# Kernel optimization log

Hardware: AMD Instinct MI355X
Metric: run time of the kernel (lower is better)

The kernel has to match this reference:

```python
import jax, jax.numpy as jnp
import numpy as np

ENERGY_PERCENT = 0.8


def setup_inputs() -> dict:
    key = jax.random.key(0)
    B, T, C = 32, 4096, 128
    x = jax.random.normal(key, (B, T, C), dtype=jnp.float32)
    return {"x": x}


def reference(x):
    # x: [B, T, C]; FFT along time axis.
    T = x.shape[1]
    xf = jnp.fft.rfft(x, axis=1)                      # [B, F, C] complex
    energies = jnp.abs(xf) ** 2                       # [B, F, C]

    # Sort energies descending along freq axis (per batch, per channel).
    sorted_indices = jnp.argsort(-energies, axis=1)   # [B, F, C] int
    sorted_energies = jnp.take_along_axis(energies, sorted_indices, axis=1)

    total_energy = jnp.sum(energies, axis=1, keepdims=True)        # [B, 1, C]
    cumulative = jnp.cumsum(sorted_energies, axis=1)               # [B, F, C]

    # Smallest k such that cumulative energy exceeds energy_percent of total.
    exceeded = cumulative > total_energy * ENERGY_PERCENT          # [B, F, C] bool
    k = jnp.argmax(exceeded, axis=1) + 1                           # [B, C]

    # rank[b, f, c] = position of frequency f in the descending energy order;
    # this is the inverse permutation of sorted_indices (argsort of a permutation).
    rank = jnp.argsort(sorted_indices, axis=1)                     # [B, F, C]

    is_low_freq = rank < k[:, None, :]                             # [B, F, C]

    # Zero out the high-energy ("low-frequency") components -> residual x_var.
    mask = jnp.where(is_low_freq, 0.0, 1.0).astype(x.dtype)        # [B, F, C]
    x_var = jnp.fft.irfft(xf * mask, n=T, axis=1)                  # [B, T, C]
    x_inv = x - x_var
    return (x_var, x_inv)
```

## Files before the change

kernel.cpp:

```cpp
#include <hip/hip_runtime.h>


#define TLEN 4096
#define N2   2048
#define CCH  128
#define BB   32
#define NSER (BB * CCH)
#define HALF 16777216
#define PI_F 3.14159265358979323846f
#define NT   64
#define TS   64
#define SLAB (CCH * TS)

#define LP(i) ((i) + ((i) >> 5))

__device__ __forceinline__ void cmul(float& r, float& i, float br, float bi) {
  float tr = r * br - i * bi;
  i = r * bi + i * br;
  r = tr;
}

__device__ __forceinline__ void dft4(float vr[4], float vi[4], float s) {
  float t0r = vr[0] + vr[2], t0i = vi[0] + vi[2];
  float t1r = vr[0] - vr[2], t1i = vi[0] - vi[2];
  float t2r = vr[1] + vr[3], t2i = vi[1] + vi[3];
  float d3r = vr[1] - vr[3], d3i = vi[1] - vi[3];
  float t3r = -s * d3i, t3i = s * d3r;
  vr[0] = t0r + t2r; vi[0] = t0i + t2i;
  vr[1] = t1r + t3r; vi[1] = t1i + t3i;
  vr[2] = t0r - t2r; vi[2] = t0i - t2i;
  vr[3] = t1r - t3r; vi[3] = t1i - t3i;
}

__device__ __forceinline__ void dft8(float vr[8], float vi[8], float s) {
  float er[4]  = {vr[0], vr[2], vr[4], vr[6]};
  float ei[4]  = {vi[0], vi[2], vi[4], vi[6]};
  float odr[4] = {vr[1], vr[3], vr[5], vr[7]};
  float odi[4] = {vi[1], vi[3], vi[5], vi[7]};
  dft4(er, ei, s);
  dft4(odr, odi, s);
  const float c = 0.70710678118654752440f;
  float wr[4] = {1.0f, c, 0.0f, -c};
  float wi[4] = {0.0f, s * c, s, s * c};
  #pragma unroll
  for (int k = 0; k < 4; ++k) {
    float tr = wr[k] * odr[k] - wi[k] * odi[k];
    float ti = wr[k] * odi[k] + wi[k] * odr[k];
    vr[k]     = er[k] + tr; vi[k]     = ei[k] + ti;
    vr[k + 4] = er[k] - tr; vi[k + 4] = ei[k] - ti;
  }
}

__device__ __forceinline__ void stage8_first(float* zr, float* zi, int tid, float s) {
  float vr[8], vi[8];
  #pragma unroll
  for (int r = 0; r < 8; ++r) {
    int idx = LP(tid + (r << 8));
    vr[r] = zr[idx]; vi[r] = zi[idx];
  }
  dft8(vr, vi, s);
  __syncthreads();
  #pragma unroll
  for (int r = 0; r < 8; ++r) {
    int idx = LP((tid << 3) + r);
    zr[idx] = vr[r]; zi[idx] = vi[r];
  }
  __syncthreads();
}

template <int NS>
__device__ __forceinline__ void stage8_tw(float* zr, float* zi, int tid, float s) {
  int j = tid;
  int p = j & (NS - 1);
  float vr[8], vi[8];
  #pragma unroll
  for (int r = 0; r < 8; ++r) {
    int idx = LP(j + (r << 8));
    vr[r] = zr[idx]; vi[r] = zi[idx];
  }
  float ang = s * 6.28318530717958647692f * (float)p / (float)(NS * 8);
  float s1, c1; __sincosf(ang, &s1, &c1);
  float c2 = c1 * c1 - s1 * s1, s2 = 2.0f * c1 * s1;
  float c3 = c2 * c1 - s2 * s1, s3 = c2 * s1 + s2 * c1;
  float c4 = c2 * c2 - s2 * s2, s4 = 2.0f * c2 * s2;
  float c5 = c4 * c1 - s4 * s1, s5 = c4 * s1 + s4 * c1;
  float c6 = c4 * c2 - s4 * s2, s6 = c4 * s2 + s4 * c2;
  float c7 = c4 * c3 - s4 * s3, s7 = c4 * s3 + s4 * c3;
  cmul(vr[1], vi[1], c1, s1);
  cmul(vr[2], vi[2], c2, s2);
  cmul(vr[3], vi[3], c3, s3);
  cmul(vr[4], vi[4], c4, s4);
  cmul(vr[5], vi[5], c5, s5);
  cmul(vr[6], vi[6], c6, s6);
  cmul(vr[7], vi[7], c7, s7);
  dft8(vr, vi, s);
  __syncthreads();
  int idxD = ((j - p) << 3) + p;
  #pragma unroll
  for (int r = 0; r < 8; ++r) {
    int idx = LP(idxD + r * NS);
    zr[idx] = vr[r]; zi[idx] = vi[r];
  }
  __syncthreads();
}

__device__ __forceinline__ void stage4_last(float* zr, float* zi, int tid, float s) {
  #pragma unroll
  for (int half = 0; half < 2; ++half) {
    int j = tid + (half << 8);
    float ang = s * PI_F * (float)j * (1.0f / 1024.0f);
    float s1, c1; __sincosf(ang, &s1, &c1);
    float c2 = c1 * c1 - s1 * s1, s2 = 2.0f * c1 * s1;
    float c3 = c2 * c1 - s2 * s1, s3 = c2 * s1 + s2 * c1;
    float vr[4], vi[4];
    #pragma unroll
    for (int r = 0; r < 4; ++r) {
      int idx = LP(j + (r << 9));
      vr[r] = zr[idx]; vi[r] = zi[idx];
    }
    cmul(vr[1], vi[1], c1, s1);
    cmul(vr[2], vi[2], c2, s2);
    cmul(vr[3], vi[3], c3, s3);
    dft4(vr, vi, s);
    #pragma unroll
    for (int r = 0; r < 4; ++r) {
      int idx = LP(j + (r << 9));
      zr[idx] = vr[r]; zi[idx] = vi[r];
    }
  }
  __syncthreads();
}

__device__ __forceinline__ void fft2048(float* zr, float* zi, int tid, float s) {
  stage8_first(zr, zi, tid, s);
  stage8_tw<8>(zr, zi, tid, s);
  stage8_tw<64>(zr, zi, tid, s);
  stage4_last(zr, zi, tid, s);
}

__device__ __forceinline__ float block_sum(float v, float* red, int tid, int bank) {
  #pragma unroll
  for (int o = 32; o > 0; o >>= 1) v += __shfl_down(v, o, 64);
  if ((tid & 63) == 0) red[(bank << 2) + (tid >> 6)] = v;
  __syncthreads();
  int b4 = bank << 2;
  return red[b4] + red[b4 + 1] + red[b4 + 2] + red[b4 + 3];
}

__global__ __launch_bounds__(256) void fourier_filter_series(float* __restrict__ buf) {
  __shared__ float zr[2113], zi[2113];
  __shared__ float red[8];
  int tid = threadIdx.x;
  int b = blockIdx.x >> 7, c = blockIdx.x & 127;
  float* bufp = buf + (size_t)b * (NT * SLAB) + (size_t)c * TS;

  #pragma unroll
  for (int j = 0; j < 8; ++j) {
    int k = tid + (j << 8);
    int off = ((k >> 5) << 13) + ((k & 31) << 1);
    float2 v = *(const float2*)(bufp + off);
    zr[LP(k)] = v.x; zi[LP(k)] = v.y;
  }
  __syncthreads();

  fft2048(zr, zi, tid, -1.0f);

  float eb[9];
  eb[8] = 0.0f;
  const float RC  = 0.92387953251128675613f;
  const float RSn = -0.38268343236508977173f;
  float ws, wc;
  __sincosf(-PI_F * (float)tid * (1.0f / 2048.0f), &ws, &wc);
  #pragma unroll
  for (int jj = 0; jj < 4; ++jj) {
    int k = tid + (jj << 8);
    int mkz = (N2 - k) & (N2 - 1);
    int ik = LP(k), im = LP(N2 - k);
    float akr = zr[ik],      aki = zi[ik];
    float bkr = zr[LP(mkz)], bki = zi[LP(mkz)];
    float Er  = 0.5f * (akr + bkr);
    float Ei  = 0.5f * (aki - bki);
    float Or_ = 0.5f * (aki + bki);
    float Oi  = 0.5f * (bkr - akr);
    float tr = wc * Or_ - ws * Oi;
    float ti = wc * Oi + ws * Or_;
    float x0r = Er + tr, x0i = Ei + ti;
    float x1r = Er - tr, x1i = ti - Ei;
    zr[ik] = x0r; zi[ik] = x0i;
    zr[im] = x1r; zi[im] = x1i;
    eb[2 * jj]     = x0r * x0r + x0i * x0i;
    eb[2 * jj + 1] = x1r * x1r + x1i * x1i;
    float nwc = wc * RC - ws * RSn;
    ws = wc * RSn + ws * RC; wc = nwc;
  }
  if (tid == 0) {
    int i4 = LP(1024);
    float re = zr[i4], im_ = zi[i4];
    zi[i4] = -im_;
    eb[8] = re * re + im_ * im_;
  }

  float tloc = 0.0f;
  #pragma unroll
  for (int s = 0; s < 9; ++s) tloc += eb[s];
  float total = block_sum(tloc, red, tid, 0);
  float thresh = 0.8f * total;

  unsigned lo = 0u, hi = 0x7F7FFFFFu;
  for (int it = 0; it < 31; ++it) {
    unsigned mid = (lo + hi + 1u) >> 1;
    float tau = __uint_as_float(mid);
    float loc = 0.0f;
    #pragma unroll
    for (int s = 0; s < 9; ++s) loc += (eb[s] >= tau) ? eb[s] : 0.0f;
    float ssum = block_sum(loc, red, tid, (it + 1) & 1);
    if (ssum > thresh) lo = mid; else hi = mid - 1;
  }
  float tau = __uint_as_float(lo);

  const float RSp = 0.38268343236508977173f;
  __sincosf(PI_F * (float)tid * (1.0f / 2048.0f), &ws, &wc);
  #pragma unroll
  for (int jj = 0; jj < 4; ++jj) {
    int k = tid + (jj << 8);
    int ik = LP(k), im = LP(N2 - k);
    float xkr = zr[ik], xki = zi[ik];
    float xmr = zr[im], xmi = zi[im];
    float ekk = xkr * xkr + xki * xki;
    float emm = xmr * xmr + xmi * xmi;
    if (ekk >= tau) { xkr = 0.0f; xki = 0.0f; }
    if (emm >= tau) { xmr = 0.0f; xmi = 0.0f; }
    float Er = 0.5f * (xkr + xmr);
    float Ei = 0.5f * (xki - xmi);
    float Br = 0.5f * (xkr - xmr);
    float Bi = 0.5f * (xki + xmi);
    float Or_ = wc * Br - ws * Bi;
    float Oi  = wc * Bi + ws * Br;
    zr[ik] = Er - Oi;  zi[ik] = Ei + Or_;
    zr[im] = Er + Oi;  zi[im] = Or_ - Ei;
    float nwc = wc * RC - ws * RSp;
    ws = wc * RSp + ws * RC; wc = nwc;
  }
  if (tid == 0) {
    int i4 = LP(1024);
    float re = zr[i4], im_ = zi[i4];
    float e = re * re + im_ * im_;
    if (e >= tau) { re = 0.0f; im_ = 0.0f; }
    zr[i4] = re; zi[i4] = -im_;
  }
  __syncthreads();

  fft2048(zr, zi, tid, 1.0f);

  const float scale = 1.0f / 2048.0f;
  #pragma unroll
  for (int j = 0; j < 8; ++j) {
    int k = tid + (j << 8);
    int off = ((k >> 5) << 13) + ((k & 31) << 1);
    float2 v;
    v.x = zr[LP(k)] * scale;
    v.y = zi[LP(k)] * scale;
    *(float2*)(bufp + off) = v;
  }
}

__global__ __launch_bounds__(512) void transpose_fwd(const float* __restrict__ x, float* __restrict__ buf) {
  __shared__ float lds[CCH * 65];
  int tb = blockIdx.x, b = blockIdx.y;
  const float* xp = x + ((size_t)b * TLEN + (size_t)tb * TS) * CCH;
  #pragma unroll
  for (int it = 0; it < 4; ++it) {
    int idx = threadIdx.x + (it << 9);
    int r = idx >> 5, c4 = (idx & 31) << 2;
    float4 v = *(const float4*)(xp + (size_t)r * CCH + c4);
    lds[(c4 + 0) * 65 + r] = v.x;
    lds[(c4 + 1) * 65 + r] = v.y;
    lds[(c4 + 2) * 65 + r] = v.z;
    lds[(c4 + 3) * 65 + r] = v.w;
  }
  __syncthreads();
  float* op = buf + ((size_t)b * NT + tb) * SLAB;
  #pragma unroll
  for (int it = 0; it < 4; ++it) {
    int idx = threadIdx.x + (it << 9);
    int c = idx >> 4, s4 = (idx & 15) << 2;
    float4 v;
    v.x = lds[c * 65 + s4 + 0];
    v.y = lds[c * 65 + s4 + 1];
    v.z = lds[c * 65 + s4 + 2];
    v.w = lds[c * 65 + s4 + 3];
    *(float4*)(op + c * TS + s4) = v;
  }
}

__global__ __launch_bounds__(512) void finalize_t(const float* __restrict__ buf, const float* __restrict__ x,
                                                  float* __restrict__ xvar, float* __restrict__ xinv) {
  __shared__ float lds[TS * 132];
  int tb = blockIdx.x, b = blockIdx.y;
  const float* ip = buf + ((size_t)b * NT + tb) * SLAB;
  #pragma unroll
  for (int it = 0; it < 4; ++it) {
    int idx = threadIdx.x + (it << 9);
    int c = idx >> 4, s4 = (idx & 15) << 2;
    float4 v = *(const float4*)(ip + c * TS + s4);
    lds[(s4 + 0) * 132 + c] = v.x;
    lds[(s4 + 1) * 132 + c] = v.y;
    lds[(s4 + 2) * 132 + c] = v.z;
    lds[(s4 + 3) * 132 + c] = v.w;
  }
  __syncthreads();
  size_t rowbase = ((size_t)b * TLEN + (size_t)tb * TS) * CCH;
  #pragma unroll
  for (int it = 0; it < 4; ++it) {
    int idx = threadIdx.x + (it << 9);
    int t = idx >> 5, c4 = (idx & 31) << 2;
    float4 v = *(const float4*)(&lds[t * 132 + c4]);
    size_t off = rowbase + (size_t)t * CCH + c4;
    float4 xv = *(const float4*)(x + off);
    *(float4*)(xvar + off) = v;
    *(float4*)(xinv + off) = make_float4(xv.x - v.x, xv.y - v.y, xv.z - v.z, xv.w - v.w);
  }
}

extern "C" void kernel_launch(void* const* d_in, const int* in_sizes, int n_in,
                              void* d_out, int out_size, void* d_ws, size_t ws_size,
                              hipStream_t stream) {
  const float* x = (const float*)d_in[0];
  float* out  = (float*)d_out;
  float* xvar = out;
  float* xinv = out + HALF;

  bool use_ws = ws_size >= (size_t)HALF * sizeof(float);
  float* buf = use_ws ? (float*)d_ws : xinv;

  dim3 tgrid(NT, BB);
  transpose_fwd<<<tgrid, 512, 0, stream>>>(x, buf);
  fourier_filter_series<<<NSER, 256, 0, stream>>>(buf);
  finalize_t<<<tgrid, 512, 0, stream>>>(buf, x, xvar, xinv);
}
```

Baseline: 300.7 us.

## Fuse transpose, FFT filter, and finalize into one kernel with quaternary threshold search

Replaces the three-kernel pipeline (transpose to a workspace, per-series FFT filter, transpose back and subtract) with one kernel. Each 512-thread block handles two channels of one batch and reads and writes x, x_var and x_inv directly with strided float2 accesses, so the intermediate buffer round trips disappear. The threshold bisection also becomes a 4-way search over three candidates per step, cutting block-wide reductions from 31 to 16. The cost is that global accesses are now 8-byte strided across time rows, which coalesces poorly, and the 512-thread blocks use more LDS each.

```diff
diff --git a/kernel.cpp b/kernel.cpp
--- a/kernel.cpp
+++ b/kernel.cpp
@@ -5,12 +5,9 @@
 #define N2   2048
 #define CCH  128
 #define BB   32
-#define NSER (BB * CCH)
 #define HALF 16777216
 #define PI_F 3.14159265358979323846f
-#define NT   64
-#define TS   64
-#define SLAB (CCH * TS)
+#define ARR  2113
 
 #define LP(i) ((i) + ((i) >> 5))
 
@@ -51,26 +48,26 @@
   }
 }
 
-__device__ __forceinline__ void stage8_first(float* zr, float* zi, int tid, float s) {
+__device__ __forceinline__ void stage8_first(float* zr, float* zi, int ctid, float s) {
   float vr[8], vi[8];
   #pragma unroll
   for (int r = 0; r < 8; ++r) {
-    int idx = LP(tid + (r << 8));
+    int idx = LP(ctid + (r << 8));
     vr[r] = zr[idx]; vi[r] = zi[idx];
   }
   dft8(vr, vi, s);
   __syncthreads();
   #pragma unroll
   for (int r = 0; r < 8; ++r) {
-    int idx = LP((tid << 3) + r);
+    int idx = LP((ctid << 3) + r);
     zr[idx] = vr[r]; zi[idx] = vi[r];
   }
   __syncthreads();
 }
 
 template <int NS>
-__device__ __forceinline__ void stage8_tw(float* zr, float* zi, int tid, float s) {
-  int j = tid;
+__device__ __forceinline__ void stage8_tw(float* zr, float* zi, int ctid, float s) {
+  int j = ctid;
   int p = j & (NS - 1);
   float vr[8], vi[8];
   #pragma unroll
@@ -104,10 +101,10 @@
   __syncthreads();
 }
 
-__device__ __forceinline__ void stage4_last(float* zr, float* zi, int tid, float s) {
+__device__ __forceinline__ void stage4_last(float* zr, float* zi, int ctid, float s) {
   #pragma unroll
   for (int half = 0; half < 2; ++half) {
-    int j = tid + (half << 8);
+    int j = ctid + (half << 8);
     float ang = s * PI_F * (float)j * (1.0f / 1024.0f);
     float s1, c1; __sincosf(ang, &s1, &c1);
     float c2 = c1 * c1 - s1 * s1, s2 = 2.0f * c1 * s1;
@@ -131,53 +128,80 @@
   __syncthreads();
 }
 
-__device__ __forceinline__ void fft2048(float* zr, float* zi, int tid, float s) {
-  stage8_first(zr, zi, tid, s);
-  stage8_tw<8>(zr, zi, tid, s);
-  stage8_tw<64>(zr, zi, tid, s);
-  stage4_last(zr, zi, tid, s);
-}
-
-__device__ __forceinline__ float block_sum(float v, float* red, int tid, int bank) {
+__device__ __forceinline__ void fft2048(float* zr, float* zi, int ctid, float s) {
+  stage8_first(zr, zi, ctid, s);
+  stage8_tw<8>(zr, zi, ctid, s);
+  stage8_tw<64>(zr, zi, ctid, s);
+  stage4_last(zr, zi, ctid, s);
+}
+
+__device__ __forceinline__ float block_sum1(float v, float* red, int tid, int ch, int bank) {
   #pragma unroll
   for (int o = 32; o > 0; o >>= 1) v += __shfl_down(v, o, 64);
-  if ((tid & 63) == 0) red[(bank << 2) + (tid >> 6)] = v;
-  __syncthreads();
-  int b4 = bank << 2;
-  return red[b4] + red[b4 + 1] + red[b4 + 2] + red[b4 + 3];
-}
-
-__global__ __launch_bounds__(256) void fourier_filter_series(float* __restrict__ buf) {
-  __shared__ float zr[2113], zi[2113];
-  __shared__ float red[8];
+  if ((tid & 63) == 0) red[((ch << 1) + bank) * 4 + ((tid >> 6) & 3)] = v;
+  __syncthreads();
+  const float* bp = red + ((ch << 1) + bank) * 4;
+  return bp[0] + bp[1] + bp[2] + bp[3];
+}
+
+__device__ __forceinline__ void block_sum3(float v[3], float* red3, int tid, int ch, int bank) {
+  #pragma unroll
+  for (int o = 32; o > 0; o >>= 1) {
+    v[0] += __shfl_down(v[0], o, 64);
+    v[1] += __shfl_down(v[1], o, 64);
+    v[2] += __shfl_down(v[2], o, 64);
+  }
+  if ((tid & 63) == 0) {
+    float* sp = red3 + (((ch << 1) + bank) * 4 + ((tid >> 6) & 3)) * 3;
+    sp[0] = v[0]; sp[1] = v[1]; sp[2] = v[2];
+  }
+  __syncthreads();
+  const float* bp = red3 + ((ch << 1) + bank) * 12;
+  v[0] = bp[0] + bp[3] + bp[6] + bp[9];
+  v[1] = bp[1] + bp[4] + bp[7] + bp[10];
+  v[2] = bp[2] + bp[5] + bp[8] + bp[11];
+}
+
+__global__ __launch_bounds__(512) void fourier_fused(const float* __restrict__ x,
+                                                     float* __restrict__ xvar,
+                                                     float* __restrict__ xinv) {
+  __shared__ float zr[2][ARR], zi[2][ARR];
+  __shared__ float red1[16];
+  __shared__ float red3[48];
   int tid = threadIdx.x;
-  int b = blockIdx.x >> 7, c = blockIdx.x & 127;
-  float* bufp = buf + (size_t)b * (NT * SLAB) + (size_t)c * TS;
-
-  #pragma unroll
-  for (int j = 0; j < 8; ++j) {
-    int k = tid + (j << 8);
-    int off = ((k >> 5) << 13) + ((k & 31) << 1);
-    float2 v = *(const float2*)(bufp + off);
-    zr[LP(k)] = v.x; zi[LP(k)] = v.y;
-  }
-  __syncthreads();
-
-  fft2048(zr, zi, tid, -1.0f);
+  int cg = blockIdx.x, b = blockIdx.y;
+  int ch = tid >> 8, ctid = tid & 255;
+  float* Zr = zr[ch];
+  float* Zi = zi[ch];
+
+  const float* xp = x + (size_t)b * TLEN * CCH + 2 * cg;
+
+  #pragma unroll
+  for (int i = 0; i < 8; ++i) {
+    int t = (i << 9) + tid;
+    float2 v = *(const float2*)(xp + (size_t)t * CCH);
+    int k = t >> 1;
+    float* base = (t & 1) ? zi[0] : zr[0];
+    base[LP(k)] = v.x;
+    base[ARR + LP(k)] = v.y;
+  }
+  __syncthreads();
+
+  fft2048(Zr, Zi, ctid, -1.0f);
 
   float eb[9];
   eb[8] = 0.0f;
   const float RC  = 0.92387953251128675613f;
   const float RSn = -0.38268343236508977173f;
   float ws, wc;
-  __sincosf(-PI_F * (float)tid * (1.0f / 2048.0f), &ws, &wc);
+  __sincosf(-PI_F * (float)ctid * (1.0f / 2048.0f), &ws, &wc);
   #pragma unroll
   for (int jj = 0; jj < 4; ++jj) {
-    int k = tid + (jj << 8);
+    int k = ctid + (jj << 8);
     int mkz = (N2 - k) & (N2 - 1);
     int ik = LP(k), im = LP(N2 - k);
-    float akr = zr[ik],      aki = zi[ik];
-    float bkr = zr[LP(mkz)], bki = zi[LP(mkz)];
+    float akr = Zr[ik],      aki = Zi[ik];
+    float bkr = Zr[LP(mkz)], bki = Zi[LP(mkz)];
     float Er  = 0.5f * (akr + bkr);
     float Ei  = 0.5f * (aki - bki);
     float Or_ = 0.5f * (aki + bki);
@@ -186,46 +210,61 @@
     float ti = wc * Oi + ws * Or_;
     float x0r = Er + tr, x0i = Ei + ti;
     float x1r = Er - tr, x1i = ti - Ei;
-    zr[ik] = x0r; zi[ik] = x0i;
-    zr[im] = x1r; zi[im] = x1i;
+    Zr[ik] = x0r; Zi[ik] = x0i;
+    Zr[im] = x1r; Zi[im] = x1i;
     eb[2 * jj]     = x0r * x0r + x0i * x0i;
     eb[2 * jj + 1] = x1r * x1r + x1i * x1i;
     float nwc = wc * RC - ws * RSn;
     ws = wc * RSn + ws * RC; wc = nwc;
   }
-  if (tid == 0) {
+  if (ctid == 0) {
     int i4 = LP(1024);
-    float re = zr[i4], im_ = zi[i4];
-    zi[i4] = -im_;
+    float re = Zr[i4], im_ = Zi[i4];
+    Zi[i4] = -im_;
     eb[8] = re * re + im_ * im_;
   }
 
   float tloc = 0.0f;
   #pragma unroll
   for (int s = 0; s < 9; ++s) tloc += eb[s];
-  float total = block_sum(tloc, red, tid, 0);
+  float total = block_sum1(tloc, red1, tid, ch, 0);
   float thresh = 0.8f * total;
 
   unsigned lo = 0u, hi = 0x7F7FFFFFu;
-  for (int it = 0; it < 31; ++it) {
-    unsigned mid = (lo + hi + 1u) >> 1;
-    float tau = __uint_as_float(mid);
-    float loc = 0.0f;
+  for (int it = 0; it < 16; ++it) {
+    unsigned span = hi - lo;
+    unsigned q = span >> 2;
+    unsigned m1 = lo + (q ? q : 1u);
+    unsigned m2 = lo + (q ? (q << 1) : 2u);
+    unsigned m3 = lo + (q ? (q * 3u) : 3u);
+    m1 = m1 > hi ? hi : m1;
+    m2 = m2 > hi ? hi : m2;
+    m3 = m3 > hi ? hi : m3;
+    float t1 = __uint_as_float(m1), t2 = __uint_as_float(m2), t3 = __uint_as_float(m3);
+    float v[3] = {0.0f, 0.0f, 0.0f};
     #pragma unroll
-    for (int s = 0; s < 9; ++s) loc += (eb[s] >= tau) ? eb[s] : 0.0f;
-    float ssum = block_sum(loc, red, tid, (it + 1) & 1);
-    if (ssum > thresh) lo = mid; else hi = mid - 1;
+    for (int s = 0; s < 9; ++s) {
+      float e = eb[s];
+      v[0] += (e >= t1) ? e : 0.0f;
+      v[1] += (e >= t2) ? e : 0.0f;
+      v[2] += (e >= t3) ? e : 0.0f;
+    }
+    block_sum3(v, red3, tid, ch, (it + 1) & 1);
+    if (v[2] > thresh)      { lo = m3; }
+    else if (v[1] > thresh) { lo = m2; hi = m3 - 1u; }
+    else if (v[0] > thresh) { lo = m1; hi = m2 - 1u; }
+    else                    { hi = m1 - 1u; }
   }
   float tau = __uint_as_float(lo);
 
   const float RSp = 0.38268343236508977173f;
-  __sincosf(PI_F * (float)tid * (1.0f / 2048.0f), &ws, &wc);
+  __sincosf(PI_F * (float)ctid * (1.0f / 2048.0f), &ws, &wc);
   #pragma unroll
   for (int jj = 0; jj < 4; ++jj) {
-    int k = tid + (jj << 8);
+    int k = ctid + (jj << 8);
     int ik = LP(k), im = LP(N2 - k);
-    float xkr = zr[ik], xki = zi[ik];
-    float xmr = zr[im], xmi = zi[im];
+    float xkr = Zr[ik], xki = Zi[ik];
+    float xmr = Zr[im], xmi = Zi[im];
     float ekk = xkr * xkr + xki * xki;
     float emm = xmr * xmr + xmi * xmi;
     if (ekk >= tau) { xkr = 0.0f; xki = 0.0f; }
@@ -236,89 +275,37 @@
     float Bi = 0.5f * (xki + xmi);
     float Or_ = wc * Br - ws * Bi;
     float Oi  = wc * Bi + ws * Br;
-    zr[ik] = Er - Oi;  zi[ik] = Ei + Or_;
-    zr[im] = Er + Oi;  zi[im] = Or_ - Ei;
+    Zr[ik] = Er - Oi;  Zi[ik] = Ei + Or_;
+    Zr[im] = Er + Oi;  Zi[im] = Or_ - Ei;
     float nwc = wc * RC - ws * RSp;
     ws = wc * RSp + ws * RC; wc = nwc;
   }
-  if (tid == 0) {
+  if (ctid == 0) {
     int i4 = LP(1024);
-    float re = zr[i4], im_ = zi[i4];
+    float re = Zr[i4], im_ = Zi[i4];
     float e = re * re + im_ * im_;
     if (e >= tau) { re = 0.0f; im_ = 0.0f; }
-    zr[i4] = re; zi[i4] = -im_;
-  }
-  __syncthreads();
-
-  fft2048(zr, zi, tid, 1.0f);
+    Zr[i4] = re; Zi[i4] = -im_;
+  }
+  __syncthreads();
+
+  fft2048(Zr, Zi, ctid, 1.0f);
 
   const float scale = 1.0f / 2048.0f;
-  #pragma unroll
-  for (int j = 0; j < 8; ++j) {
-    int k = tid + (j << 8);
-    int off = ((k >> 5) << 13) + ((k & 31) << 1);
-    float2 v;
-    v.x = zr[LP(k)] * scale;
-    v.y = zi[LP(k)] * scale;
-    *(float2*)(bufp + off) = v;
-  }
-}
-
-__global__ __launch_bounds__(512) void transpose_fwd(const float* __restrict__ x, float* __restrict__ buf) {
-  __shared__ float lds[CCH * 65];
-  int tb = blockIdx.x, b = blockIdx.y;
-  const float* xp = x + ((size_t)b * TLEN + (size_t)tb * TS) * CCH;
-  #pragma unroll
-  for (int it = 0; it < 4; ++it) {
-    int idx = threadIdx.x + (it << 9);
-    int r = idx >> 5, c4 = (idx & 31) << 2;
-    float4 v = *(const float4*)(xp + (size_t)r * CCH + c4);
-    lds[(c4 + 0) * 65 + r] = v.x;
-    lds[(c4 + 1) * 65 + r] = v.y;
-    lds[(c4 + 2) * 65 + r] = v.z;
-    lds[(c4 + 3) * 65 + r] = v.w;
-  }
-  __syncthreads();
-  float* op = buf + ((size_t)b * NT + tb) * SLAB;
-  #pragma unroll
-  for (int it = 0; it < 4; ++it) {
-    int idx = threadIdx.x + (it << 9);
-    int c = idx >> 4, s4 = (idx & 15) << 2;
-    float4 v;
-    v.x = lds[c * 65 + s4 + 0];
-    v.y = lds[c * 65 + s4 + 1];
-    v.z = lds[c * 65 + s4 + 2];
-    v.w = lds[c * 65 + s4 + 3];
-    *(float4*)(op + c * TS + s4) = v;
-  }
-}
-
-__global__ __launch_bounds__(512) void finalize_t(const float* __restrict__ buf, const float* __restrict__ x,
-                                                  float* __restrict__ xvar, float* __restrict__ xinv) {
-  __shared__ float lds[TS * 132];
-  int tb = blockIdx.x, b = blockIdx.y;
-  const float* ip = buf + ((size_t)b * NT + tb) * SLAB;
-  #pragma unroll
-  for (int it = 0; it < 4; ++it) {
-    int idx = threadIdx.x + (it << 9);
-    int c = idx >> 4, s4 = (idx & 15) << 2;
-    float4 v = *(const float4*)(ip + c * TS + s4);
-    lds[(s4 + 0) * 132 + c] = v.x;
-    lds[(s4 + 1) * 132 + c] = v.y;
-    lds[(s4 + 2) * 132 + c] = v.z;
-    lds[(s4 + 3) * 132 + c] = v.w;
-  }
-  __syncthreads();
-  size_t rowbase = ((size_t)b * TLEN + (size_t)tb * TS) * CCH;
-  #pragma unroll
-  for (int it = 0; it < 4; ++it) {
-    int idx = threadIdx.x + (it << 9);
-    int t = idx >> 5, c4 = (idx & 31) << 2;
-    float4 v = *(const float4*)(&lds[t * 132 + c4]);
-    size_t off = rowbase + (size_t)t * CCH + c4;
-    float4 xv = *(const float4*)(x + off);
-    *(float4*)(xvar + off) = v;
-    *(float4*)(xinv + off) = make_float4(xv.x - v.x, xv.y - v.y, xv.z - v.z, xv.w - v.w);
+  float* vo = xvar + (size_t)b * TLEN * CCH + 2 * cg;
+  float* io = xinv + (size_t)b * TLEN * CCH + 2 * cg;
+  #pragma unroll
+  for (int i = 0; i < 8; ++i) {
+    int t = (i << 9) + tid;
+    int k = t >> 1;
+    const float* base = (t & 1) ? zi[0] : zr[0];
+    float a0 = base[LP(k)] * scale;
+    float a1 = base[ARR + LP(k)] * scale;
+    float2 xv = *(const float2*)(xp + (size_t)t * CCH);
+    float2 v0; v0.x = a0;        v0.y = a1;
+    float2 v1; v1.x = xv.x - a0; v1.y = xv.y - a1;
+    *(float2*)(vo + (size_t)t * CCH) = v0;
+    *(float2*)(io + (size_t)t * CCH) = v1;
   }
 }
 
@@ -330,11 +317,6 @@
   float* xvar = out;
   float* xinv = out + HALF;
 
-  bool use_ws = ws_size >= (size_t)HALF * sizeof(float);
-  float* buf = use_ws ? (float*)d_ws : xinv;
-
-  dim3 tgrid(NT, BB);
-  transpose_fwd<<<tgrid, 512, 0, stream>>>(x, buf);
-  fourier_filter_series<<<NSER, 256, 0, stream>>>(buf);
-  finalize_t<<<tgrid, 512, 0, stream>>>(buf, x, xvar, xinv);
-}
+  dim3 grid(CCH / 2, BB);
+  fourier_fused<<<grid, 512, 0, stream>>>(x, xvar, xinv);
+}
```

After: 558.2 us. 85.6% more time.
